# Performance work log

Hardware: AMD Instinct MI355X
Metric: run time of the kernel (lower is better)

## Reference

```python
import jax, jax.numpy as jnp
import numpy as np

RADIUS = 12
SIGMA = 5.0
USM_LO, USM_HI = 0.0, 5.0
BEGIN = 0  # cfg.usm_begin_param


def _gauss_kernel_2d():
    x = jnp.arange(-RADIUS, RADIUS + 1, dtype=jnp.float32)
    k = jnp.exp(-0.5 * (x / SIGMA) ** 2)
    k = k / k.sum()
    return jnp.outer(k, k)  # [25, 25]


def setup_inputs() -> dict:
    key = jax.random.key(0)
    k1, k2 = jax.random.split(key)
    img = jax.random.uniform(k1, (16, 3, 512, 512), dtype=jnp.float32)
    features = jax.random.normal(k2, (16, 8), dtype=jnp.float32)
    return {"img": img, "features": features}


def reference(img, features):
    p = features[:, BEGIN:BEGIN + 1]                       # [B, 1]
    param = (jnp.tanh(p) * 0.5 + 0.5) * (USM_HI - USM_LO) + USM_LO

    # depthwise 25x25 gaussian blur with reflect padding
    kernel = jnp.broadcast_to(_gauss_kernel_2d(), (3, 1, 25, 25))  # OIHW, groups=3
    padded = jnp.pad(img, ((0, 0), (0, 0), (RADIUS, RADIUS), (RADIUS, RADIUS)),
                     mode='reflect')
    blurred = jax.lax.conv_general_dilated(
        padded, kernel, window_strides=(1, 1), padding='VALID',
        dimension_numbers=('NCHW', 'OIHW', 'NCHW'), feature_group_count=3)

    out = img + param.reshape(-1, 1, 1, 1) * (img - blurred)
    return out, param
```

## Files before the change

### kernel.cpp

```cpp
#include <hip/hip_runtime.h>
#include <hip/hip_fp16.h>


#define RADIUS 12
#define KS     25
#define TILE   64
#define PT     (TILE + 2 * RADIUS)
#define TA_LD  104
#define IMG_W  512
#define IMG_H  512
#define PLANE  (IMG_W * IMG_H)
#define NPLANE 48

#define N_STAGE (PT * 11)
#define N_H     (PT * (TILE / 8))

__device__ __constant__ float GW[KS] = {
    0.00453456f, 0.00718308f, 0.01093238f, 0.01598625f, 0.02245983f,
    0.03031760f, 0.03931982f, 0.04899550f, 0.05865827f, 0.06747307f,
    0.07456928f, 0.07918039f, 0.08077993f, 0.07918039f, 0.07456928f,
    0.06747307f, 0.05865827f, 0.04899550f, 0.03931982f, 0.03031760f,
    0.02245983f, 0.01598625f, 0.01093238f, 0.00718308f, 0.00453456f
};

__device__ __forceinline__ int reflect512(int i) {
    i = (i < 0) ? -i : i;
    return (i >= 512) ? (1022 - i) : i;
}

typedef _Float16 h2_t __attribute__((ext_vector_type(2)));

__device__ __forceinline__ unsigned h2u(__half2 h) {
    union { __half2 h; unsigned u; } x; x.h = h; return x.u;
}
__device__ __forceinline__ float u_lo(unsigned u) {
    union { unsigned u; __half2 h; } x; x.u = u;
    return __half2float(__low2half(x.h));
}
__device__ __forceinline__ float u_hi(unsigned u) {
    union { unsigned u; __half2 h; } x; x.u = u;
    return __half2float(__high2half(x.h));
}

#if __has_builtin(__builtin_amdgcn_fdot2)
__device__ __forceinline__ float fdot2u(unsigned a, unsigned b, float c) {
    union { unsigned u; h2_t h; } ua, ub;
    ua.u = a; ub.u = b;
    return __builtin_amdgcn_fdot2(ua.h, ub.h, c, false);
}
#else
__device__ __forceinline__ float fdot2u(unsigned a, unsigned b, float c) {
    return c + u_lo(a) * u_lo(b) + u_hi(a) * u_hi(b);
}
#endif

__device__ __forceinline__ uint4 h_slot(const __half (*tA)[TA_LD], int py, int g,
                                        const unsigned* W2, unsigned WE, unsigned WO) {
    const uint4 qa = *(const uint4*)&tA[py][g * 8];
    const uint4 qb = *(const uint4*)&tA[py][g * 8 + 8];
    const uint4 qc = *(const uint4*)&tA[py][g * 8 + 16];
    const uint4 qd = *(const uint4*)&tA[py][g * 8 + 24];

    unsigned P[16] = { qa.x, qa.y, qa.z, qa.w, qb.x, qb.y, qb.z, qb.w,
                       qc.x, qc.y, qc.z, qc.w, qd.x, qd.y, qd.z, qd.w };
    unsigned S[15];
#pragma unroll
    for (int i = 0; i < 15; ++i)
        S[i] = __builtin_amdgcn_alignbit(P[i + 1], P[i], 16);

    float acc[8];
#pragma unroll
    for (int h = 0; h < 4; ++h) {
        float a = 0.f;
#pragma unroll
        for (int m = 0; m < 12; ++m) a = fdot2u(P[h + m], W2[m], a);
        acc[2 * h] = fdot2u(P[h + 12], WE, a);
    }
#pragma unroll
    for (int h = 0; h < 4; ++h) {
        float a = 0.f;
#pragma unroll
        for (int m = 0; m < 12; ++m) a = fdot2u(S[h + m], W2[m], a);
        acc[2 * h + 1] = fdot2u(P[h + 12], WO, a);
    }

    uint4 pk;
    pk.x = h2u(__floats2half2_rn(acc[0], acc[1]));
    pk.y = h2u(__floats2half2_rn(acc[2], acc[3]));
    pk.z = h2u(__floats2half2_rn(acc[4], acc[5]));
    pk.w = h2u(__floats2half2_rn(acc[6], acc[7]));
    return pk;
}

__global__ __launch_bounds__(256) void usm_fused_kernel(
    const float* __restrict__ img, const float* __restrict__ feat,
    float* __restrict__ out, float* __restrict__ out_param)
{
    __shared__ __half tileA[PT][TA_LD];

    const int tid = threadIdx.x;
    const int tx0 = blockIdx.x * TILE, ty0 = blockIdx.y * TILE;
    const int zc = blockIdx.z, b = zc / 3;
    const float param = (tanhf(feat[b * 8]) * 0.5f + 0.5f) * 5.0f;
    const float* __restrict__ src = img + (size_t)zc * PLANE;
    const bool xedge = (blockIdx.x == 0) || (blockIdx.x == 7);

    unsigned W2[12];
#pragma unroll
    for (int m = 0; m < 12; ++m)
        W2[m] = h2u(__floats2half2_rn(GW[2 * m], GW[2 * m + 1]));
    const unsigned WE = h2u(__floats2half2_rn(GW[24], 0.f));
    const unsigned WO = h2u(__floats2half2_rn(0.f, GW[24]));

#pragma unroll
    for (int it = 0; it < 4; ++it) {
        const int li = tid + it * 256;
        if (it < 3 || li < N_STAGE) {
            const int py = li / 11, s = li - py * 11;
            const int gy = reflect512(ty0 - RADIUS + py);
            const float* __restrict__ rowp = src + (size_t)gy * IMG_W;
            const int gx = tx0 - RADIUS + s * 8;
            float4 va, vb;
            if (!xedge) {
                va = *(const float4*)(rowp + gx);
                vb = *(const float4*)(rowp + gx + 4);
            } else {
                va.x = rowp[reflect512(gx)];     va.y = rowp[reflect512(gx + 1)];
                va.z = rowp[reflect512(gx + 2)]; va.w = rowp[reflect512(gx + 3)];
                vb.x = rowp[reflect512(gx + 4)]; vb.y = rowp[reflect512(gx + 5)];
                vb.z = rowp[reflect512(gx + 6)]; vb.w = rowp[reflect512(gx + 7)];
            }
            uint4 pk;
            pk.x = h2u(__floats2half2_rn(va.x, va.y));
            pk.y = h2u(__floats2half2_rn(va.z, va.w));
            pk.z = h2u(__floats2half2_rn(vb.x, vb.y));
            pk.w = h2u(__floats2half2_rn(vb.z, vb.w));
            *(uint4*)&tileA[py][s * 8] = pk;
        }
    }
    __syncthreads();

    const int li1 = tid + 256, li2 = tid + 512;
    const bool act2 = (li2 < N_H);
    uint4 h0 = h_slot(tileA, tid >> 3, tid & 7, W2, WE, WO);
    uint4 h1 = h_slot(tileA, li1 >> 3, li1 & 7, W2, WE, WO);
    uint4 h2w = act2 ? h_slot(tileA, li2 >> 3, li2 & 7, W2, WE, WO)
                     : make_uint4(0, 0, 0, 0);
    __syncthreads();

    *(uint4*)&tileA[tid >> 3][(tid & 7) * 8] = h0;
    *(uint4*)&tileA[li1 >> 3][(li1 & 7) * 8] = h1;
    if (act2) *(uint4*)&tileA[li2 >> 3][(li2 & 7) * 8] = h2w;
    __syncthreads();

    const int tx4 = (tid & 15) * 4, ry0 = (tid >> 4) * 4;
    float ax[4], ay[4], az[4], aw[4];
#pragma unroll
    for (int d = 0; d < 4; ++d) ax[d] = ay[d] = az[d] = aw[d] = 0.f;

#pragma unroll
    for (int k = 0; k < KS + 3; ++k) {
        uint2 rd = *(const uint2*)&tileA[ry0 + k][tx4];
        const float c0 = u_lo(rd.x), c1 = u_hi(rd.x);
        const float c2 = u_lo(rd.y), c3 = u_hi(rd.y);
#pragma unroll
        for (int d = 0; d < 4; ++d) {
            const int kk = k - d;
            if (kk >= 0 && kk < KS) {
                const float wk = GW[kk];
                ax[d] += wk * c0; ay[d] += wk * c1;
                az[d] += wk * c2; aw[d] += wk * c3;
            }
        }
    }

    float* __restrict__ dst = out + (size_t)zc * PLANE;
#pragma unroll
    for (int d = 0; d < 4; ++d) {
        const int oy = ty0 + ry0 + d;
        float4 v = *(const float4*)(src + (size_t)oy * IMG_W + tx0 + tx4);
        float4 o;
        o.x = v.x + param * (v.x - ax[d]);
        o.y = v.y + param * (v.y - ay[d]);
        o.z = v.z + param * (v.z - az[d]);
        o.w = v.w + param * (v.w - aw[d]);
        *(float4*)(dst + (size_t)oy * IMG_W + tx0 + tx4) = o;
    }

    if (tid == 0 && blockIdx.x == 0 && blockIdx.y == 0 && (zc - b * 3) == 0)
        out_param[b] = param;
}

extern "C" void kernel_launch(void* const* d_in, const int* in_sizes, int n_in,
                              void* d_out, int out_size, void* d_ws, size_t ws_size,
                              hipStream_t stream) {
    const float* img  = (const float*)d_in[0];
    const float* feat = (const float*)d_in[1];
    float* out       = (float*)d_out;
    float* out_param = (float*)d_out + (size_t)NPLANE * PLANE;

    usm_fused_kernel<<<dim3(8, 8, NPLANE), 256, 0, stream>>>(img, feat, out, out_param);
}
```

Baseline: 42.19 us.

## Process four planes per block with register prefetch of next plane's tile

Each block now handles four consecutive image planes instead of one. While it computes the blur for the current plane, it loads the next plane's halo tile from global memory into registers, then writes it to shared memory after the current plane is done. The goal is to hide global load latency behind compute. The cost is more registers held live and more barriers, and the grid shrinks from 3072 to 768 blocks, which lowers the parallelism available on a GPU with many CUs.

```diff
diff --git a/kernel.cpp b/kernel.cpp
--- a/kernel.cpp
+++ b/kernel.cpp
@@ -11,6 +11,7 @@
 #define IMG_H  512
 #define PLANE  (IMG_W * IMG_H)
 #define NPLANE 48
+#define ZPB    4
 
 #define N_STAGE (PT * 11)
 #define N_H     (PT * (TILE / 8))
@@ -54,64 +55,10 @@
 }
 #endif
 
-__device__ __forceinline__ uint4 h_slot(const __half (*tA)[TA_LD], int py, int g,
-                                        const unsigned* W2, unsigned WE, unsigned WO) {
-    const uint4 qa = *(const uint4*)&tA[py][g * 8];
-    const uint4 qb = *(const uint4*)&tA[py][g * 8 + 8];
-    const uint4 qc = *(const uint4*)&tA[py][g * 8 + 16];
-    const uint4 qd = *(const uint4*)&tA[py][g * 8 + 24];
-
-    unsigned P[16] = { qa.x, qa.y, qa.z, qa.w, qb.x, qb.y, qb.z, qb.w,
-                       qc.x, qc.y, qc.z, qc.w, qd.x, qd.y, qd.z, qd.w };
-    unsigned S[15];
-#pragma unroll
-    for (int i = 0; i < 15; ++i)
-        S[i] = __builtin_amdgcn_alignbit(P[i + 1], P[i], 16);
-
-    float acc[8];
-#pragma unroll
-    for (int h = 0; h < 4; ++h) {
-        float a = 0.f;
-#pragma unroll
-        for (int m = 0; m < 12; ++m) a = fdot2u(P[h + m], W2[m], a);
-        acc[2 * h] = fdot2u(P[h + 12], WE, a);
-    }
-#pragma unroll
-    for (int h = 0; h < 4; ++h) {
-        float a = 0.f;
-#pragma unroll
-        for (int m = 0; m < 12; ++m) a = fdot2u(S[h + m], W2[m], a);
-        acc[2 * h + 1] = fdot2u(P[h + 12], WO, a);
-    }
-
-    uint4 pk;
-    pk.x = h2u(__floats2half2_rn(acc[0], acc[1]));
-    pk.y = h2u(__floats2half2_rn(acc[2], acc[3]));
-    pk.z = h2u(__floats2half2_rn(acc[4], acc[5]));
-    pk.w = h2u(__floats2half2_rn(acc[6], acc[7]));
-    return pk;
-}
-
-__global__ __launch_bounds__(256) void usm_fused_kernel(
-    const float* __restrict__ img, const float* __restrict__ feat,
-    float* __restrict__ out, float* __restrict__ out_param)
+__device__ __forceinline__ void stage_issue(
+    const float* __restrict__ src, int tid, int tx0, int ty0, bool xedge,
+    float4* pva, float4* pvb)
 {
-    __shared__ __half tileA[PT][TA_LD];
-
-    const int tid = threadIdx.x;
-    const int tx0 = blockIdx.x * TILE, ty0 = blockIdx.y * TILE;
-    const int zc = blockIdx.z, b = zc / 3;
-    const float param = (tanhf(feat[b * 8]) * 0.5f + 0.5f) * 5.0f;
-    const float* __restrict__ src = img + (size_t)zc * PLANE;
-    const bool xedge = (blockIdx.x == 0) || (blockIdx.x == 7);
-
-    unsigned W2[12];
-#pragma unroll
-    for (int m = 0; m < 12; ++m)
-        W2[m] = h2u(__floats2half2_rn(GW[2 * m], GW[2 * m + 1]));
-    const unsigned WE = h2u(__floats2half2_rn(GW[24], 0.f));
-    const unsigned WO = h2u(__floats2half2_rn(0.f, GW[24]));
-
 #pragma unroll
     for (int it = 0; it < 4; ++it) {
         const int li = tid + it * 256;
@@ -120,75 +67,171 @@
             const int gy = reflect512(ty0 - RADIUS + py);
             const float* __restrict__ rowp = src + (size_t)gy * IMG_W;
             const int gx = tx0 - RADIUS + s * 8;
-            float4 va, vb;
             if (!xedge) {
-                va = *(const float4*)(rowp + gx);
-                vb = *(const float4*)(rowp + gx + 4);
+                pva[it] = *(const float4*)(rowp + gx);
+                pvb[it] = *(const float4*)(rowp + gx + 4);
             } else {
+                float4 va, vb;
                 va.x = rowp[reflect512(gx)];     va.y = rowp[reflect512(gx + 1)];
                 va.z = rowp[reflect512(gx + 2)]; va.w = rowp[reflect512(gx + 3)];
                 vb.x = rowp[reflect512(gx + 4)]; vb.y = rowp[reflect512(gx + 5)];
                 vb.z = rowp[reflect512(gx + 6)]; vb.w = rowp[reflect512(gx + 7)];
+                pva[it] = va; pvb[it] = vb;
             }
+        }
+    }
+}
+
+__device__ __forceinline__ void stage_write(
+    __half (*tA)[TA_LD], int tid, const float4* pva, const float4* pvb)
+{
+#pragma unroll
+    for (int it = 0; it < 4; ++it) {
+        const int li = tid + it * 256;
+        if (it < 3 || li < N_STAGE) {
+            const int py = li / 11, s = li - py * 11;
             uint4 pk;
-            pk.x = h2u(__floats2half2_rn(va.x, va.y));
-            pk.y = h2u(__floats2half2_rn(va.z, va.w));
-            pk.z = h2u(__floats2half2_rn(vb.x, vb.y));
-            pk.w = h2u(__floats2half2_rn(vb.z, vb.w));
-            *(uint4*)&tileA[py][s * 8] = pk;
-        }
-    }
+            pk.x = h2u(__floats2half2_rn(pva[it].x, pva[it].y));
+            pk.y = h2u(__floats2half2_rn(pva[it].z, pva[it].w));
+            pk.z = h2u(__floats2half2_rn(pvb[it].x, pvb[it].y));
+            pk.w = h2u(__floats2half2_rn(pvb[it].z, pvb[it].w));
+            *(uint4*)&tA[py][s * 8] = pk;
+        }
+    }
+}
+
+__device__ __forceinline__ uint4 h_slot(const __half (*tA)[TA_LD], int py, int g,
+                                        const unsigned* W2, unsigned WE, unsigned WO) {
+    const uint4 qa = *(const uint4*)&tA[py][g * 8];
+    const uint4 qb = *(const uint4*)&tA[py][g * 8 + 8];
+    const uint4 qc = *(const uint4*)&tA[py][g * 8 + 16];
+    const uint4 qd = *(const uint4*)&tA[py][g * 8 + 24];
+
+    unsigned P[16] = { qa.x, qa.y, qa.z, qa.w, qb.x, qb.y, qb.z, qb.w,
+                       qc.x, qc.y, qc.z, qc.w, qd.x, qd.y, qd.z, qd.w };
+    unsigned S[15];
+#pragma unroll
+    for (int i = 0; i < 15; ++i)
+        S[i] = __builtin_amdgcn_alignbit(P[i + 1], P[i], 16);
+
+    float acc[8];
+#pragma unroll
+    for (int h = 0; h < 4; ++h) {
+        float a = 0.f;
+#pragma unroll
+        for (int m = 0; m < 12; ++m) a = fdot2u(P[h + m], W2[m], a);
+        acc[2 * h] = fdot2u(P[h + 12], WE, a);
+    }
+#pragma unroll
+    for (int h = 0; h < 4; ++h) {
+        float a = 0.f;
+#pragma unroll
+        for (int m = 0; m < 12; ++m) a = fdot2u(S[h + m], W2[m], a);
+        acc[2 * h + 1] = fdot2u(P[h + 12], WO, a);
+    }
+
+    uint4 pk;
+    pk.x = h2u(__floats2half2_rn(acc[0], acc[1]));
+    pk.y = h2u(__floats2half2_rn(acc[2], acc[3]));
+    pk.z = h2u(__floats2half2_rn(acc[4], acc[5]));
+    pk.w = h2u(__floats2half2_rn(acc[6], acc[7]));
+    return pk;
+}
+
+__global__ __launch_bounds__(256) void usm_fused_kernel(
+    const float* __restrict__ img, const float* __restrict__ feat,
+    float* __restrict__ out, float* __restrict__ out_param)
+{
+    __shared__ __half tileA[PT][TA_LD];
+
+    const int tid = threadIdx.x;
+    const int tx0 = blockIdx.x * TILE, ty0 = blockIdx.y * TILE;
+    const int z0  = blockIdx.z * ZPB;
+    const bool xedge = (blockIdx.x == 0) || (blockIdx.x == 7);
+
+    unsigned W2[12];
+#pragma unroll
+    for (int m = 0; m < 12; ++m)
+        W2[m] = h2u(__floats2half2_rn(GW[2 * m], GW[2 * m + 1]));
+    const unsigned WE = h2u(__floats2half2_rn(GW[24], 0.f));
+    const unsigned WO = h2u(__floats2half2_rn(0.f, GW[24]));
+
+    const int tx4 = (tid & 15) * 4, ry0 = (tid >> 4) * 4;
+
+    float4 pva[4], pvb[4];
+    stage_issue(img + (size_t)z0 * PLANE, tid, tx0, ty0, xedge, pva, pvb);
+    stage_write(tileA, tid, pva, pvb);
     __syncthreads();
 
-    const int li1 = tid + 256, li2 = tid + 512;
-    const bool act2 = (li2 < N_H);
-    uint4 h0 = h_slot(tileA, tid >> 3, tid & 7, W2, WE, WO);
-    uint4 h1 = h_slot(tileA, li1 >> 3, li1 & 7, W2, WE, WO);
-    uint4 h2w = act2 ? h_slot(tileA, li2 >> 3, li2 & 7, W2, WE, WO)
-                     : make_uint4(0, 0, 0, 0);
-    __syncthreads();
-
-    *(uint4*)&tileA[tid >> 3][(tid & 7) * 8] = h0;
-    *(uint4*)&tileA[li1 >> 3][(li1 & 7) * 8] = h1;
-    if (act2) *(uint4*)&tileA[li2 >> 3][(li2 & 7) * 8] = h2w;
-    __syncthreads();
-
-    const int tx4 = (tid & 15) * 4, ry0 = (tid >> 4) * 4;
-    float ax[4], ay[4], az[4], aw[4];
-#pragma unroll
-    for (int d = 0; d < 4; ++d) ax[d] = ay[d] = az[d] = aw[d] = 0.f;
-
-#pragma unroll
-    for (int k = 0; k < KS + 3; ++k) {
-        uint2 rd = *(const uint2*)&tileA[ry0 + k][tx4];
-        const float c0 = u_lo(rd.x), c1 = u_hi(rd.x);
-        const float c2 = u_lo(rd.y), c3 = u_hi(rd.y);
+    for (int t = 0; t < ZPB; ++t) {
+        const int zc = z0 + t;
+        const int b  = zc / 3;
+        const float* __restrict__ src = img + (size_t)zc * PLANE;
+
+        if (t + 1 < ZPB)
+            stage_issue(src + PLANE, tid, tx0, ty0, xedge, pva, pvb);
+
+        float4 cv0 = *(const float4*)(src + (size_t)(ty0 + ry0 + 0) * IMG_W + tx0 + tx4);
+        float4 cv1 = *(const float4*)(src + (size_t)(ty0 + ry0 + 1) * IMG_W + tx0 + tx4);
+        float4 cv2 = *(const float4*)(src + (size_t)(ty0 + ry0 + 2) * IMG_W + tx0 + tx4);
+        float4 cv3 = *(const float4*)(src + (size_t)(ty0 + ry0 + 3) * IMG_W + tx0 + tx4);
+
+        const float param = (tanhf(feat[b * 8]) * 0.5f + 0.5f) * 5.0f;
+
+        const int li1 = tid + 256, li2 = tid + 512;
+        const bool act2 = (li2 < N_H);
+        uint4 h0 = h_slot(tileA, tid >> 3, tid & 7, W2, WE, WO);
+        uint4 h1 = h_slot(tileA, li1 >> 3, li1 & 7, W2, WE, WO);
+        uint4 h2w = act2 ? h_slot(tileA, li2 >> 3, li2 & 7, W2, WE, WO)
+                         : make_uint4(0, 0, 0, 0);
+        __syncthreads();
+
+        *(uint4*)&tileA[tid >> 3][(tid & 7) * 8] = h0;
+        *(uint4*)&tileA[li1 >> 3][(li1 & 7) * 8] = h1;
+        if (act2) *(uint4*)&tileA[li2 >> 3][(li2 & 7) * 8] = h2w;
+        __syncthreads();
+
+        float ax[4], ay[4], az[4], aw[4];
+#pragma unroll
+        for (int d = 0; d < 4; ++d) ax[d] = ay[d] = az[d] = aw[d] = 0.f;
+
+#pragma unroll
+        for (int k = 0; k < KS + 3; ++k) {
+            uint2 rd = *(const uint2*)&tileA[ry0 + k][tx4];
+            const float c0 = u_lo(rd.x), c1 = u_hi(rd.x);
+            const float c2 = u_lo(rd.y), c3 = u_hi(rd.y);
+#pragma unroll
+            for (int d = 0; d < 4; ++d) {
+                const int kk = k - d;
+                if (kk >= 0 && kk < KS) {
+                    const float wk = GW[kk];
+                    ax[d] += wk * c0; ay[d] += wk * c1;
+                    az[d] += wk * c2; aw[d] += wk * c3;
+                }
+            }
+        }
+
+        float* __restrict__ dst = out + (size_t)zc * PLANE;
 #pragma unroll
         for (int d = 0; d < 4; ++d) {
-            const int kk = k - d;
-            if (kk >= 0 && kk < KS) {
-                const float wk = GW[kk];
-                ax[d] += wk * c0; ay[d] += wk * c1;
-                az[d] += wk * c2; aw[d] += wk * c3;
-            }
-        }
-    }
-
-    float* __restrict__ dst = out + (size_t)zc * PLANE;
-#pragma unroll
-    for (int d = 0; d < 4; ++d) {
-        const int oy = ty0 + ry0 + d;
-        float4 v = *(const float4*)(src + (size_t)oy * IMG_W + tx0 + tx4);
-        float4 o;
-        o.x = v.x + param * (v.x - ax[d]);
-        o.y = v.y + param * (v.y - ay[d]);
-        o.z = v.z + param * (v.z - az[d]);
-        o.w = v.w + param * (v.w - aw[d]);
-        *(float4*)(dst + (size_t)oy * IMG_W + tx0 + tx4) = o;
-    }
-
-    if (tid == 0 && blockIdx.x == 0 && blockIdx.y == 0 && (zc - b * 3) == 0)
-        out_param[b] = param;
+            const float4 v = (d == 0) ? cv0 : (d == 1) ? cv1 : (d == 2) ? cv2 : cv3;
+            float4 o;
+            o.x = v.x + param * (v.x - ax[d]);
+            o.y = v.y + param * (v.y - ay[d]);
+            o.z = v.z + param * (v.z - az[d]);
+            o.w = v.w + param * (v.w - aw[d]);
+            *(float4*)(dst + (size_t)(ty0 + ry0 + d) * IMG_W + tx0 + tx4) = o;
+        }
+
+        if (tid == 0 && blockIdx.x == 0 && blockIdx.y == 0 && (zc - b * 3) == 0)
+            out_param[b] = param;
+
+        if (t + 1 < ZPB) {
+            __syncthreads();
+            stage_write(tileA, tid, pva, pvb);
+            __syncthreads();
+        }
+    }
 }
 
 extern "C" void kernel_launch(void* const* d_in, const int* in_sizes, int n_in,
@@ -199,5 +242,5 @@
     float* out       = (float*)d_out;
     float* out_param = (float*)d_out + (size_t)NPLANE * PLANE;
 
-    usm_fused_kernel<<<dim3(8, 8, NPLANE), 256, 0, stream>>>(img, feat, out, out_param);
-}
+    usm_fused_kernel<<<dim3(8, 8, NPLANE / ZPB), 256, 0, stream>>>(img, feat, out, out_param);
+}
```

New measurement: 47.19 us. 11.8% more time.
